# Kernel tuning notes

Hardware: AMD Instinct MI355X
Metric: run time of the kernel (lower is better)

The kernel has to match this reference:

```python
import jax, jax.numpy as jnp
import numpy as np

B, T, C, H = 8, 2048, 1024, 64  # batch, seq_len, num_embed, size_head


def setup_inputs() -> dict:
    key = jax.random.key(0)
    kx, kq, kk, kv = jax.random.split(key, 4)
    return {
        "x": jax.random.normal(kx, (B, T, C), dtype=jnp.float32),
        "Wq": jax.random.normal(kq, (C, H), dtype=jnp.float32) * 0.02,
        "Wk": jax.random.normal(kk, (C, H), dtype=jnp.float32) * 0.02,
        "Wv": jax.random.normal(kv, (C, H), dtype=jnp.float32) * 0.02,
    }


def reference(x, Wq, Wk, Wv):
    # x: [B, T, C]; single-head causal self-attention.
    # NOTE: original scales by num_channels = x.shape[-1] (= C), not head dim.
    num_channels = x.shape[-1]
    q = jnp.einsum("btc,ch->bth", x, Wq)
    k = jnp.einsum("btc,ch->bth", x, Wk)
    v = jnp.einsum("btc,ch->bth", x, Wv)
    w = jnp.einsum("bqh,bkh->bqk", q, k) * (num_channels ** -0.5)  # [B,T,T]
    causal = jnp.tril(jnp.ones((x.shape[1], x.shape[1]), dtype=bool))
    w = jnp.where(causal, w, -jnp.inf)
    w = jax.nn.softmax(w, axis=-1)
    # dropout is identity in eval/reference mode
    out = jnp.einsum("bqk,bkh->bqh", w, v)  # [B,T,H]
    return out
```

## Files before the change

kernel.cpp:

```cpp
#include <hip/hip_runtime.h>
#include <hip/hip_bf16.h>
#include <stdint.h>

#define Bn 8
#define Tn 2048
#define Cn 1024
#define Hn 64

typedef __attribute__((ext_vector_type(8))) short bf16x8;
typedef __attribute__((ext_vector_type(4))) short bf16x4;
typedef __attribute__((ext_vector_type(4))) float f32x4;

#if defined(__HIP_DEVICE_COMPILE__) && !__has_builtin(__builtin_amdgcn_mfma_f32_16x16x16bf16_1k)
#error "mfma_f32_16x16x16bf16_1k required on gfx950"
#endif
#define MFMA16(a, b, c) __builtin_amdgcn_mfma_f32_16x16x16bf16_1k(a, b, c, 0, 0, 0)
#define MFMA32(a, b, c) __builtin_amdgcn_mfma_f32_16x16x32_bf16(a, b, c, 0, 0, 0)

__device__ __forceinline__ unsigned short f2bf(float f) {
  union { float f; unsigned int u; } v; v.f = f;
  unsigned int u = v.u;
  u = u + 0x7fffu + ((u >> 16) & 1u);
  return (unsigned short)(u >> 16);
}

__device__ __forceinline__ void gload16(const void* g, void* l) {
  __builtin_amdgcn_global_load_lds(
      (const __attribute__((address_space(1))) unsigned int*)g,
      (__attribute__((address_space(3))) unsigned int*)l, 16, 0, 0);
}

__global__ __launch_bounds__(256) void k_prep(const float* __restrict__ Wq,
                                              const float* __restrict__ Wk,
                                              const float* __restrict__ Wv,
                                              unsigned short* __restrict__ Wt) {
  const int m = blockIdx.x >> 6;
  const int h = blockIdx.x & 63;
  const float* W = (m == 0) ? Wq : (m == 1) ? Wk : Wv;
  const int tid = threadIdx.x;
  unsigned short* dst = Wt + ((size_t)(m * 64 + h)) * 1024;
#pragma unroll
  for (int j = 0; j < 4; ++j) {
    int c = j * 256 + tid;
    dst[c] = f2bf(W[(size_t)c * 64 + h]);
  }
}

__global__ __launch_bounds__(256, 2) void k_qkv(const float* __restrict__ x,
                                                const unsigned short* __restrict__ Wt,
                                                unsigned short* __restrict__ Q,
                                                unsigned short* __restrict__ K,
                                                unsigned short* __restrict__ Vt) {
  __shared__ __align__(16) char smem[32256];
  unsigned short (*xs)[72] = (unsigned short (*)[72])smem;
  unsigned short (*wsh)[72] = (unsigned short (*)[72])(smem + 32 * 72 * 2);
  unsigned short (*os)[200] = (unsigned short (*)[200])smem;

  const int tid = threadIdx.x;
  const int lane = tid & 63;
  const int wid = tid >> 6;
  const int wm = wid >> 1, wn = wid & 1;
  const int l15 = lane & 15, g = lane >> 4;
  const int r0 = blockIdx.x * 32;

  f32x4 acc[6];
#pragma unroll
  for (int j = 0; j < 6; ++j)
#pragma unroll
    for (int r = 0; r < 4; ++r) acc[j][r] = 0.f;

  const int srow = tid >> 3;
  const int scol = (tid & 7) * 8;

  for (int kt = 0; kt < 16; ++kt) {
    const int k0 = kt * 64;
    const float* xp = x + (size_t)(r0 + srow) * 1024 + k0 + scol;
    {
      float4 v0 = *(const float4*)xp;
      float4 v1 = *(const float4*)(xp + 4);
      ushort4 b0, b1;
      b0.x = f2bf(v0.x); b0.y = f2bf(v0.y); b0.z = f2bf(v0.z); b0.w = f2bf(v0.w);
      b1.x = f2bf(v1.x); b1.y = f2bf(v1.y); b1.z = f2bf(v1.z); b1.w = f2bf(v1.w);
      *(ushort4*)&xs[srow][scol] = b0;
      *(ushort4*)&xs[srow][scol + 4] = b1;
    }
#pragma unroll
    for (int j = 0; j < 6; ++j) {
      int u = j * 256 + tid;
      int row = u >> 3, ch = u & 7;
      uint4 w = *(const uint4*)(Wt + (size_t)row * 1024 + k0 + ch * 8);
      *(uint4*)&wsh[row][ch * 8] = w;
    }
    __syncthreads();
#pragma unroll
    for (int kf = 0; kf < 2; ++kf) {
      bf16x8 a = *(const bf16x8*)&xs[wm * 16 + l15][kf * 32 + g * 8];
#pragma unroll
      for (int nf = 0; nf < 6; ++nf) {
        bf16x8 bfr = *(const bf16x8*)&wsh[wn * 96 + nf * 16 + l15][kf * 32 + g * 8];
        acc[nf] = MFMA32(a, bfr, acc[nf]);
      }
    }
    __syncthreads();
  }

#pragma unroll
  for (int nf = 0; nf < 6; ++nf)
#pragma unroll
    for (int r = 0; r < 4; ++r)
      os[wm * 16 + 4 * g + r][wn * 96 + nf * 16 + l15] = f2bf(acc[nf][r]);
  __syncthreads();

  const int b = r0 >> 11;
  const int t0 = r0 & 2047;
  {
    int row = tid >> 3, ch = tid & 7;
    *(uint4*)(Q + (size_t)(r0 + row) * 64 + ch * 8) = *(const uint4*)&os[row][ch * 8];
    *(uint4*)(K + (size_t)(r0 + row) * 64 + ch * 8) = *(const uint4*)&os[row][64 + ch * 8];
  }
  {
    int h = tid >> 2, tc = (tid & 3) * 8;
    unsigned short tmp[8];
#pragma unroll
    for (int r = 0; r < 8; ++r) tmp[r] = os[tc + r][128 + h];
    *(uint4*)(Vt + ((size_t)b * 64 + h) * 2048 + t0 + tc) = *(const uint4*)tmp;
  }
}

__global__ __launch_bounds__(256, 3) void k_attn_coop(const unsigned short* __restrict__ Q,
                                                      const unsigned short* __restrict__ K,
                                                      const unsigned short* __restrict__ Vt,
                                                      float* __restrict__ out,
                                                      float* __restrict__ po,
                                                      float* __restrict__ pml) {
  __shared__ __align__(16) unsigned short lds[2][8192];

  const int tid = threadIdx.x;
  const int lane = tid & 63;
  const int l15 = lane & 15, g = lane >> 4;
  const int wid = __builtin_amdgcn_readfirstlane(tid >> 6);

  const int raw = blockIdx.x;
  const int bi = (raw & 7) * 144 + (raw >> 3);
  const int b = bi / 144;
  const int id = bi - b * 144;
  int gq = 0;
#pragma unroll
  for (int t = 1; t < 8; ++t)
    if (id >= 2 * t * (t + 1)) gq = t;
  const int rem = id - 2 * gq * (gq + 1);
  const int ql = rem / (gq + 1);
  const int s = rem - ql * (gq + 1);
  const int qt = 4 * gq + ql;
  const int qblk = qt * 64;
  const int klo = 256 * s;
  const int khi = min(klo + 256, qblk + 64);
  const int nt = (khi - klo + 63) >> 6;
  const int q0w = qblk + wid * 16;

  const unsigned short* Qb = Q + (size_t)b * Tn * Hn;
  const unsigned short* Kb = K + (size_t)b * Tn * Hn;
  const unsigned short* Vb = Vt + (size_t)b * Hn * Tn;

  bf16x8 bq0 = *(const bf16x8*)(Qb + (size_t)(q0w + l15) * 64 + g * 8);
  bf16x8 bq1 = *(const bf16x8*)(Qb + (size_t)(q0w + l15) * 64 + 32 + g * 8);

  f32x4 o[4];
#pragma unroll
  for (int hf = 0; hf < 4; ++hf)
#pragma unroll
    for (int r = 0; r < 4; ++r) o[hf][r] = 0.f;
  float m = -1e30f, lsum = 0.f;
  const float sc = 0.03125f * 1.44269504088896f;

  auto stage = [&](int buf, int k0) {
    unsigned short* tb = &lds[buf][0];
#pragma unroll
    for (int j = 0; j < 4; ++j) {
      const int p = wid * 256 + j * 64 + lane;
      const unsigned short* src;
      if (wid < 2) {
        const int row = p >> 3, c = p & 7;
        src = Kb + (size_t)(k0 + row) * 64 + ((c ^ (row & 7)) * 8);
      } else {
        const int q = p - 512;
        const int h = q >> 3, c = q & 7;
        src = Vb + (size_t)h * Tn + k0 + ((c ^ (h & 7)) * 8);
      }
      gload16(src, tb + wid * 2048 + j * 512);
    }
  };

  stage(0, klo);
  __syncthreads();

  for (int t = 0; t < nt; ++t) {
    const int cur = t & 1;
    const int k0 = klo + t * 64;
    if (t + 1 < nt) stage(cur ^ 1, klo + (t + 1) * 64);

    const unsigned short* kt = &lds[cur][0];
    const unsigned short* vt = &lds[cur][4096];

    f32x4 sacc[4];
#pragma unroll
    for (int kc = 0; kc < 4; ++kc) {
      const int row = kc * 16 + l15;
      const int sw = row & 7;
      bf16x8 ka = *(const bf16x8*)&kt[row * 64 + ((g ^ sw) * 8)];
      bf16x8 kb2 = *(const bf16x8*)&kt[row * 64 + (((4 + g) ^ sw) * 8)];
#pragma unroll
      for (int r = 0; r < 4; ++r) sacc[kc][r] = 0.f;
      sacc[kc] = MFMA32(ka, bq0, sacc[kc]);
      sacc[kc] = MFMA32(kb2, bq1, sacc[kc]);
    }
    float sv[4][4];
    if (k0 + 63 > q0w) {
      const int q = q0w + l15;
#pragma unroll
      for (int kc = 0; kc < 4; ++kc)
#pragma unroll
        for (int r = 0; r < 4; ++r) {
          int key = k0 + kc * 16 + 4 * g + r;
          sv[kc][r] = (key <= q) ? sacc[kc][r] * sc : -1e30f;
        }
    } else {
#pragma unroll
      for (int kc = 0; kc < 4; ++kc)
#pragma unroll
        for (int r = 0; r < 4; ++r) sv[kc][r] = sacc[kc][r] * sc;
    }
    float pm = sv[0][0];
#pragma unroll
    for (int kc = 0; kc < 4; ++kc)
#pragma unroll
      for (int r = 0; r < 4; ++r) pm = fmaxf(pm, sv[kc][r]);
    if (__any(pm > m + 8.f)) {
      pm = fmaxf(pm, __shfl_xor(pm, 16));
      pm = fmaxf(pm, __shfl_xor(pm, 32));
      float mn = fmaxf(m, pm);
      float alpha = exp2f(m - mn);
      lsum *= alpha;
      float an[4];
#pragma unroll
      for (int r = 0; r < 4; ++r) an[r] = __shfl(alpha, 4 * g + r);
#pragma unroll
      for (int hf = 0; hf < 4; ++hf)
#pragma unroll
        for (int r = 0; r < 4; ++r) o[hf][r] *= an[r];
      m = mn;
    }
    float ts = 0.f;
#pragma unroll
    for (int kc = 0; kc < 4; ++kc)
#pragma unroll
      for (int r = 0; r < 4; ++r) { sv[kc][r] = exp2f(sv[kc][r] - m); ts += sv[kc][r]; }
    ts += __shfl_xor(ts, 16);
    ts += __shfl_xor(ts, 32);
    lsum += ts;
    bf16x4 pa[4];
#pragma unroll
    for (int kc = 0; kc < 4; ++kc) {
      pa[kc][0] = (short)f2bf(sv[kc][0]); pa[kc][1] = (short)f2bf(sv[kc][1]);
      pa[kc][2] = (short)f2bf(sv[kc][2]); pa[kc][3] = (short)f2bf(sv[kc][3]);
    }
    bf16x4 vf[4][4];
#pragma unroll
    for (int hf = 0; hf < 4; ++hf) {
      const int h = hf * 16 + l15, hs = h & 7;
#pragma unroll
      for (int kc = 0; kc < 4; ++kc) {
        const int gran = (kc * 2 + (g >> 1)) ^ hs;
        vf[hf][kc] = *(const bf16x4*)&vt[h * 64 + gran * 8 + (g & 1) * 4];
      }
    }
#pragma unroll
    for (int hf = 0; hf < 4; ++hf)
#pragma unroll
      for (int kc = 0; kc < 4; ++kc)
        o[hf] = MFMA16(pa[kc], vf[hf][kc], o[hf]);

    __syncthreads();
  }

  if (qt >= 4) {
    const int slot = b * 140 + id - 4;
    float* pob = po + (size_t)slot * 4096;
#pragma unroll
    for (int hf = 0; hf < 4; ++hf)
#pragma unroll
      for (int r = 0; r < 4; ++r)
        pob[(16 * wid + 4 * g + r) * 64 + hf * 16 + l15] = o[hf][r];
    if (lane < 16) {
      pml[(size_t)slot * 128 + 16 * wid + l15] = m;
      pml[(size_t)slot * 128 + 64 + 16 * wid + l15] = lsum;
    }
  } else {
    const float il = 1.f / lsum;
    float iln[4];
#pragma unroll
    for (int r = 0; r < 4; ++r) iln[r] = __shfl(il, 4 * g + r);
    float* ob = out + ((size_t)b * Tn + q0w) * 64;
#pragma unroll
    for (int hf = 0; hf < 4; ++hf)
#pragma unroll
      for (int r = 0; r < 4; ++r)
        ob[(size_t)(4 * g + r) * 64 + hf * 16 + l15] = o[hf][r] * iln[r];
  }
}

__global__ __launch_bounds__(256) void k_comb(const float* __restrict__ po,
                                              const float* __restrict__ pml,
                                              float* __restrict__ out) {
  const int qt = 4 + blockIdx.x;
  const int b = blockIdx.y;
  const int gq = qt >> 2, ql = qt & 3;
  const int nseg = gq + 1;
  const int base = b * 140 + 2 * gq * (gq + 1) + ql * (gq + 1) - 4;
  const int r = threadIdx.x >> 2;
  const int cg = threadIdx.x & 3;

  float mv[8], lv[8], M = -1e30f;
#pragma unroll
  for (int s = 0; s < 8; ++s)
    if (s < nseg) {
      mv[s] = pml[(size_t)(base + s) * 128 + r];
      lv[s] = pml[(size_t)(base + s) * 128 + 64 + r];
      M = fmaxf(M, mv[s]);
    }
  float w[8], L = 0.f;
#pragma unroll
  for (int s = 0; s < 8; ++s)
    if (s < nseg) { w[s] = exp2f(mv[s] - M); L += w[s] * lv[s]; }

  float acc[16];
#pragma unroll
  for (int c = 0; c < 16; ++c) acc[c] = 0.f;
#pragma unroll
  for (int s = 0; s < 8; ++s)
    if (s < nseg) {
      const float* pb = po + (size_t)(base + s) * 4096 + r * 64 + cg * 16;
#pragma unroll
      for (int j = 0; j < 4; ++j) {
        float4 v = *(const float4*)(pb + 4 * j);
        acc[4 * j + 0] += w[s] * v.x; acc[4 * j + 1] += w[s] * v.y;
        acc[4 * j + 2] += w[s] * v.z; acc[4 * j + 3] += w[s] * v.w;
      }
    }
  const float invL = 1.f / L;
  float* ob = out + ((size_t)b * Tn + qt * 64 + r) * 64 + cg * 16;
#pragma unroll
  for (int j = 0; j < 4; ++j) {
    float4 v;
    v.x = acc[4 * j + 0] * invL; v.y = acc[4 * j + 1] * invL;
    v.z = acc[4 * j + 2] * invL; v.w = acc[4 * j + 3] * invL;
    *(float4*)(ob + 4 * j) = v;
  }
}

__global__ __launch_bounds__(256, 2) void k_attn_wave(const unsigned short* __restrict__ Q,
                                                      const unsigned short* __restrict__ K,
                                                      const unsigned short* __restrict__ Vt,
                                                      float* __restrict__ out) {
  const int tid = threadIdx.x;
  const int lane = tid & 63;
  const int l15 = lane & 15, g = lane >> 4;
  const int wid = tid >> 6;
  const int task = blockIdx.x * 4 + wid;
  const int b = task >> 7, qt = task & 127;
  const int q0 = qt * 16;
  const int nt = (q0 + 16 + 63) >> 6;

  const unsigned short* Qb = Q + (size_t)b * Tn * Hn;
  const unsigned short* Kb = K + (size_t)b * Tn * Hn;
  const unsigned short* Vb = Vt + (size_t)b * Hn * Tn;

  bf16x8 bq0 = *(const bf16x8*)(Qb + (size_t)(q0 + l15) * 64 + g * 8);
  bf16x8 bq1 = *(const bf16x8*)(Qb + (size_t)(q0 + l15) * 64 + 32 + g * 8);

  f32x4 o[4];
#pragma unroll
  for (int hf = 0; hf < 4; ++hf)
#pragma unroll
    for (int r = 0; r < 4; ++r) o[hf][r] = 0.f;
  float m = -1e30f, lsum = 0.f;
  const float sc = 0.03125f * 1.44269504088896f;

  for (int t = 0; t < nt; ++t) {
    const int k0 = t * 64;
    bf16x4 vf[4][4];
#pragma unroll
    for (int hf = 0; hf < 4; ++hf) {
      const unsigned short* vrow = Vb + (size_t)(hf * 16 + l15) * Tn + k0 + 4 * g;
#pragma unroll
      for (int kc = 0; kc < 4; ++kc) vf[hf][kc] = *(const bf16x4*)(vrow + kc * 16);
    }
    f32x4 sacc[4];
#pragma unroll
    for (int kc = 0; kc < 4; ++kc) {
      const unsigned short* kp = Kb + (size_t)(k0 + kc * 16 + l15) * 64 + g * 8;
      bf16x8 ka = *(const bf16x8*)kp;
      bf16x8 kb2 = *(const bf16x8*)(kp + 32);
#pragma unroll
      for (int r = 0; r < 4; ++r) sacc[kc][r] = 0.f;
      sacc[kc] = MFMA32(ka, bq0, sacc[kc]);
      sacc[kc] = MFMA32(kb2, bq1, sacc[kc]);
    }
    float sv[4][4];
    if (k0 + 63 > q0) {
      const int q = q0 + l15;
#pragma unroll
      for (int kc = 0; kc < 4; ++kc)
#pragma unroll
        for (int r = 0; r < 4; ++r) {
          int key = k0 + kc * 16 + 4 * g + r;
          sv[kc][r] = (key <= q) ? sacc[kc][r] * sc : -1e30f;
        }
    } else {
#pragma unroll
      for (int kc = 0; kc < 4; ++kc)
#pragma unroll
        for (int r = 0; r < 4; ++r) sv[kc][r] = sacc[kc][r] * sc;
    }
    float pm = sv[0][0];
#pragma unroll
    for (int kc = 0; kc < 4; ++kc)
#pragma unroll
      for (int r = 0; r < 4; ++r) pm = fmaxf(pm, sv[kc][r]);
    if (__any(pm > m + 8.f)) {
      pm = fmaxf(pm, __shfl_xor(pm, 16));
      pm = fmaxf(pm, __shfl_xor(pm, 32));
      float mn = fmaxf(m, pm);
      float alpha = exp2f(m - mn);
      lsum *= alpha;
      float an[4];
#pragma unroll
      for (int r = 0; r < 4; ++r) an[r] = __shfl(alpha, 4 * g + r);
#pragma unroll
      for (int hf = 0; hf < 4; ++hf)
#pragma unroll
        for (int r = 0; r < 4; ++r) o[hf][r] *= an[r];
      m = mn;
    }
    float ts = 0.f;
#pragma unroll
    for (int kc = 0; kc < 4; ++kc)
#pragma unroll
      for (int r = 0; r < 4; ++r) { sv[kc][r] = exp2f(sv[kc][r] - m); ts += sv[kc][r]; }
    ts += __shfl_xor(ts, 16);
    ts += __shfl_xor(ts, 32);
    lsum += ts;
    bf16x4 pa[4];
#pragma unroll
    for (int kc = 0; kc < 4; ++kc) {
      pa[kc][0] = (short)f2bf(sv[kc][0]); pa[kc][1] = (short)f2bf(sv[kc][1]);
      pa[kc][2] = (short)f2bf(sv[kc][2]); pa[kc][3] = (short)f2bf(sv[kc][3]);
    }
#pragma unroll
    for (int hf = 0; hf < 4; ++hf)
#pragma unroll
      for (int kc = 0; kc < 4; ++kc)
        o[hf] = MFMA16(pa[kc], vf[hf][kc], o[hf]);
  }
  const float il = 1.f / lsum;
  float iln[4];
#pragma unroll
  for (int r = 0; r < 4; ++r) iln[r] = __shfl(il, 4 * g + r);
  float* ob = out + ((size_t)b * Tn + q0) * 64;
#pragma unroll
  for (int hf = 0; hf < 4; ++hf)
#pragma unroll
    for (int r = 0; r < 4; ++r)
      ob[(size_t)(4 * g + r) * 64 + hf * 16 + l15] = o[hf][r] * iln[r];
}

extern "C" void kernel_launch(void* const* d_in, const int* in_sizes, int n_in,
                              void* d_out, int out_size, void* d_ws, size_t ws_size,
                              hipStream_t stream) {
  const float* x  = (const float*)d_in[0];
  const float* Wq = (const float*)d_in[1];
  const float* Wk = (const float*)d_in[2];
  const float* Wv = (const float*)d_in[3];
  float* out = (float*)d_out;

  unsigned short* Wt = (unsigned short*)d_ws;
  unsigned short* Qs = Wt + 3 * 64 * 1024;
  unsigned short* Ks = Qs + (size_t)Bn * Tn * Hn;
  unsigned short* Vt = Ks + (size_t)Bn * Tn * Hn;
  const size_t bf_bytes = (3 * 64 * 1024 + 3 * (size_t)Bn * Tn * Hn) * 2;
  float* po = (float*)((char*)d_ws + bf_bytes);

  const size_t nslots = (size_t)Bn * 140;
  float* pml = po + nslots * 4096;
  const size_t need = bf_bytes + nslots * (4096 + 128) * sizeof(float);

  hipLaunchKernelGGL(k_prep, dim3(192), dim3(256), 0, stream, Wq, Wk, Wv, Wt);
  hipLaunchKernelGGL(k_qkv, dim3(512), dim3(256), 0, stream, x, Wt, Qs, Ks, Vt);
  if (ws_size >= need) {
    hipLaunchKernelGGL(k_attn_coop, dim3(1152), dim3(256), 0, stream, Qs, Ks, Vt, out, po, pml);
    hipLaunchKernelGGL(k_comb, dim3(28, 8), dim3(256), 0, stream, po, pml, out);
  } else {
    hipLaunchKernelGGL(k_attn_wave, dim3(256), dim3(256), 0, stream, Qs, Ks, Vt, out);
  }
}
```

Before: 54.93 us.

## Load QKV projection operands directly from global memory into MFMA registers

The QKV projection kernel no longer stages x and weight tiles through shared memory with two barriers per k-step. Each wave instead reads its MFMA fragments straight from global memory, converts x to bf16 in registers, and computes a 32x48 output tile over a fully unrolled k loop. This is meant to remove LDS traffic and synchronisation. In exchange, each x row is now read by all four waves, so global and L2 traffic goes up. The fragment loads are also strided and less coalesced.

```diff
diff --git a/kernel.cpp b/kernel.cpp
--- a/kernel.cpp
+++ b/kernel.cpp
@@ -51,64 +51,62 @@
                                                 unsigned short* __restrict__ Q,
                                                 unsigned short* __restrict__ K,
                                                 unsigned short* __restrict__ Vt) {
-  __shared__ __align__(16) char smem[32256];
-  unsigned short (*xs)[72] = (unsigned short (*)[72])smem;
-  unsigned short (*wsh)[72] = (unsigned short (*)[72])(smem + 32 * 72 * 2);
-  unsigned short (*os)[200] = (unsigned short (*)[200])smem;
+  __shared__ __align__(16) unsigned short os[32][200];
 
   const int tid = threadIdx.x;
   const int lane = tid & 63;
   const int wid = tid >> 6;
-  const int wm = wid >> 1, wn = wid & 1;
   const int l15 = lane & 15, g = lane >> 4;
   const int r0 = blockIdx.x * 32;
 
-  f32x4 acc[6];
-#pragma unroll
-  for (int j = 0; j < 6; ++j)
-#pragma unroll
-    for (int r = 0; r < 4; ++r) acc[j][r] = 0.f;
-
-  const int srow = tid >> 3;
-  const int scol = (tid & 7) * 8;
-
-  for (int kt = 0; kt < 16; ++kt) {
-    const int k0 = kt * 64;
-    const float* xp = x + (size_t)(r0 + srow) * 1024 + k0 + scol;
-    {
-      float4 v0 = *(const float4*)xp;
-      float4 v1 = *(const float4*)(xp + 4);
-      ushort4 b0, b1;
-      b0.x = f2bf(v0.x); b0.y = f2bf(v0.y); b0.z = f2bf(v0.z); b0.w = f2bf(v0.w);
-      b1.x = f2bf(v1.x); b1.y = f2bf(v1.y); b1.z = f2bf(v1.z); b1.w = f2bf(v1.w);
-      *(ushort4*)&xs[srow][scol] = b0;
-      *(ushort4*)&xs[srow][scol + 4] = b1;
-    }
-#pragma unroll
-    for (int j = 0; j < 6; ++j) {
-      int u = j * 256 + tid;
-      int row = u >> 3, ch = u & 7;
-      uint4 w = *(const uint4*)(Wt + (size_t)row * 1024 + k0 + ch * 8);
-      *(uint4*)&wsh[row][ch * 8] = w;
-    }
-    __syncthreads();
-#pragma unroll
-    for (int kf = 0; kf < 2; ++kf) {
-      bf16x8 a = *(const bf16x8*)&xs[wm * 16 + l15][kf * 32 + g * 8];
-#pragma unroll
-      for (int nf = 0; nf < 6; ++nf) {
-        bf16x8 bfr = *(const bf16x8*)&wsh[wn * 96 + nf * 16 + l15][kf * 32 + g * 8];
-        acc[nf] = MFMA32(a, bfr, acc[nf]);
-      }
-    }
-    __syncthreads();
-  }
-
-#pragma unroll
-  for (int nf = 0; nf < 6; ++nf)
-#pragma unroll
-    for (int r = 0; r < 4; ++r)
-      os[wm * 16 + 4 * g + r][wn * 96 + nf * 16 + l15] = f2bf(acc[nf][r]);
+  f32x4 acc[2][3];
+#pragma unroll
+  for (int mf = 0; mf < 2; ++mf)
+#pragma unroll
+    for (int nf = 0; nf < 3; ++nf)
+#pragma unroll
+      for (int r = 0; r < 4; ++r) acc[mf][nf][r] = 0.f;
+
+  const float* xr0 = x + (size_t)(r0 + l15) * 1024 + g * 8;
+  const float* xr1 = x + (size_t)(r0 + 16 + l15) * 1024 + g * 8;
+  const unsigned short* wr0 = Wt + (size_t)(wid * 48 + l15) * 1024 + g * 8;
+  const unsigned short* wr1 = wr0 + 16 * 1024;
+  const unsigned short* wr2 = wr0 + 32 * 1024;
+
+#pragma unroll
+  for (int ks = 0; ks < 32; ++ks) {
+    const int k0 = ks * 32;
+    float4 a0l = *(const float4*)(xr0 + k0);
+    float4 a0h = *(const float4*)(xr0 + k0 + 4);
+    float4 a1l = *(const float4*)(xr1 + k0);
+    float4 a1h = *(const float4*)(xr1 + k0 + 4);
+    bf16x8 a0, a1;
+    a0[0] = (short)f2bf(a0l.x); a0[1] = (short)f2bf(a0l.y);
+    a0[2] = (short)f2bf(a0l.z); a0[3] = (short)f2bf(a0l.w);
+    a0[4] = (short)f2bf(a0h.x); a0[5] = (short)f2bf(a0h.y);
+    a0[6] = (short)f2bf(a0h.z); a0[7] = (short)f2bf(a0h.w);
+    a1[0] = (short)f2bf(a1l.x); a1[1] = (short)f2bf(a1l.y);
+    a1[2] = (short)f2bf(a1l.z); a1[3] = (short)f2bf(a1l.w);
+    a1[4] = (short)f2bf(a1h.x); a1[5] = (short)f2bf(a1h.y);
+    a1[6] = (short)f2bf(a1h.z); a1[7] = (short)f2bf(a1h.w);
+    bf16x8 b0 = *(const bf16x8*)(wr0 + k0);
+    bf16x8 b1 = *(const bf16x8*)(wr1 + k0);
+    bf16x8 b2 = *(const bf16x8*)(wr2 + k0);
+    acc[0][0] = MFMA32(a0, b0, acc[0][0]);
+    acc[0][1] = MFMA32(a0, b1, acc[0][1]);
+    acc[0][2] = MFMA32(a0, b2, acc[0][2]);
+    acc[1][0] = MFMA32(a1, b0, acc[1][0]);
+    acc[1][1] = MFMA32(a1, b1, acc[1][1]);
+    acc[1][2] = MFMA32(a1, b2, acc[1][2]);
+  }
+
+#pragma unroll
+  for (int mf = 0; mf < 2; ++mf)
+#pragma unroll
+    for (int nf = 0; nf < 3; ++nf)
+#pragma unroll
+      for (int r = 0; r < 4; ++r)
+        os[mf * 16 + 4 * g + r][wid * 48 + nf * 16 + l15] = f2bf(acc[mf][nf][r]);
   __syncthreads();
 
   const int b = r0 >> 11;
```

Result: slower. 86.57 us (+57.6%).

## Double-buffer QKV projection with larger 64-row tiles and swizzled async W loads

Applied to the files above, without the earlier changes.

Restructures the QKV projection kernel to use 512-thread blocks over 64 rows with a 128-wide K step. Each wave now computes a 2x3 MFMA fragment grid instead of 1x6. X and W tiles are double-buffered in a large LDS allocation. The next tile's W is staged with direct global-to-LDS loads using an XOR swizzle against bank conflicts, overlapping loads with the current MFMAs. This halves the number of blocks and repeated W fetches, at the cost of one block per CU and heavy LDS use.

```diff
diff --git a/kernel.cpp b/kernel.cpp
--- a/kernel.cpp
+++ b/kernel.cpp
@@ -46,69 +46,97 @@
   }
 }
 
-__global__ __launch_bounds__(256, 2) void k_qkv(const float* __restrict__ x,
+__global__ __launch_bounds__(512, 1) void k_qkv(const float* __restrict__ x,
                                                 const unsigned short* __restrict__ Wt,
                                                 unsigned short* __restrict__ Q,
                                                 unsigned short* __restrict__ K,
                                                 unsigned short* __restrict__ Vt) {
-  __shared__ __align__(16) char smem[32256];
-  unsigned short (*xs)[72] = (unsigned short (*)[72])smem;
-  unsigned short (*wsh)[72] = (unsigned short (*)[72])(smem + 32 * 72 * 2);
-  unsigned short (*os)[200] = (unsigned short (*)[200])smem;
+  __shared__ __align__(16) char smem[133120];
 
   const int tid = threadIdx.x;
   const int lane = tid & 63;
-  const int wid = tid >> 6;
-  const int wm = wid >> 1, wn = wid & 1;
+  const int wid = __builtin_amdgcn_readfirstlane(tid >> 6);
+  const int wm = wid >> 2, wn = wid & 3;
   const int l15 = lane & 15, g = lane >> 4;
-  const int r0 = blockIdx.x * 32;
-
-  f32x4 acc[6];
-#pragma unroll
-  for (int j = 0; j < 6; ++j)
-#pragma unroll
-    for (int r = 0; r < 4; ++r) acc[j][r] = 0.f;
-
-  const int srow = tid >> 3;
-  const int scol = (tid & 7) * 8;
-
-  for (int kt = 0; kt < 16; ++kt) {
-    const int k0 = kt * 64;
-    const float* xp = x + (size_t)(r0 + srow) * 1024 + k0 + scol;
-    {
-      float4 v0 = *(const float4*)xp;
-      float4 v1 = *(const float4*)(xp + 4);
-      ushort4 b0, b1;
-      b0.x = f2bf(v0.x); b0.y = f2bf(v0.y); b0.z = f2bf(v0.z); b0.w = f2bf(v0.w);
-      b1.x = f2bf(v1.x); b1.y = f2bf(v1.y); b1.z = f2bf(v1.z); b1.w = f2bf(v1.w);
-      *(ushort4*)&xs[srow][scol] = b0;
-      *(ushort4*)&xs[srow][scol + 4] = b1;
-    }
+  const int r0 = blockIdx.x * 64;
+
+  f32x4 acc[2][3];
+#pragma unroll
+  for (int mf = 0; mf < 2; ++mf)
+#pragma unroll
+    for (int nf = 0; nf < 3; ++nf)
+#pragma unroll
+      for (int r = 0; r < 4; ++r) acc[mf][nf][r] = 0.f;
+
+  auto stageW = [&](int buf, int kt) {
+    char* wl = smem + 34816 + buf * 49152;
+    const int k0 = kt * 128;
 #pragma unroll
     for (int j = 0; j < 6; ++j) {
-      int u = j * 256 + tid;
-      int row = u >> 3, ch = u & 7;
-      uint4 w = *(const uint4*)(Wt + (size_t)row * 1024 + k0 + ch * 8);
-      *(uint4*)&wsh[row][ch * 8] = w;
+      const int cidx = wid + j * 8;
+      const int row = cidx * 4 + (lane >> 4);
+      const int lg = (lane & 15) ^ (row & 15);
+      gload16(Wt + (size_t)row * 1024 + k0 + lg * 8, wl + cidx * 1024);
+    }
+  };
+  auto stageX = [&](int buf, int kt) {
+    unsigned short (*xs)[136] = (unsigned short (*)[136])(smem + buf * 17408);
+    const int row = tid >> 3;
+    const int c0 = (tid & 7) * 16;
+    const float* xp = x + (size_t)(r0 + row) * 1024 + kt * 128 + c0;
+    float4 v0 = *(const float4*)xp;
+    float4 v1 = *(const float4*)(xp + 4);
+    float4 v2 = *(const float4*)(xp + 8);
+    float4 v3 = *(const float4*)(xp + 12);
+    ushort4 b0, b1, b2, b3;
+    b0.x = f2bf(v0.x); b0.y = f2bf(v0.y); b0.z = f2bf(v0.z); b0.w = f2bf(v0.w);
+    b1.x = f2bf(v1.x); b1.y = f2bf(v1.y); b1.z = f2bf(v1.z); b1.w = f2bf(v1.w);
+    b2.x = f2bf(v2.x); b2.y = f2bf(v2.y); b2.z = f2bf(v2.z); b2.w = f2bf(v2.w);
+    b3.x = f2bf(v3.x); b3.y = f2bf(v3.y); b3.z = f2bf(v3.z); b3.w = f2bf(v3.w);
+    *(ushort4*)&xs[row][c0] = b0;
+    *(ushort4*)&xs[row][c0 + 4] = b1;
+    *(ushort4*)&xs[row][c0 + 8] = b2;
+    *(ushort4*)&xs[row][c0 + 12] = b3;
+  };
+
+  stageW(0, 0);
+  stageX(0, 0);
+  __syncthreads();
+
+  for (int kt = 0; kt < 8; ++kt) {
+    const int cur = kt & 1;
+    if (kt < 7) {
+      stageW(cur ^ 1, kt + 1);
+      stageX(cur ^ 1, kt + 1);
+    }
+    const unsigned short (*xs)[136] =
+        (const unsigned short (*)[136])(smem + cur * 17408);
+    const unsigned short* wl = (const unsigned short*)(smem + 34816 + cur * 49152);
+#pragma unroll
+    for (int ks = 0; ks < 4; ++ks) {
+      bf16x8 a0 = *(const bf16x8*)&xs[wm * 32 + l15][ks * 32 + g * 8];
+      bf16x8 a1 = *(const bf16x8*)&xs[wm * 32 + 16 + l15][ks * 32 + g * 8];
+#pragma unroll
+      for (int nf = 0; nf < 3; ++nf) {
+        const int row = wn * 48 + nf * 16 + l15;
+        const int phys = (ks * 4 + g) ^ (row & 15);
+        bf16x8 b = *(const bf16x8*)&wl[row * 128 + phys * 8];
+        acc[0][nf] = MFMA32(a0, b, acc[0][nf]);
+        acc[1][nf] = MFMA32(a1, b, acc[1][nf]);
+      }
     }
     __syncthreads();
-#pragma unroll
-    for (int kf = 0; kf < 2; ++kf) {
-      bf16x8 a = *(const bf16x8*)&xs[wm * 16 + l15][kf * 32 + g * 8];
-#pragma unroll
-      for (int nf = 0; nf < 6; ++nf) {
-        bf16x8 bfr = *(const bf16x8*)&wsh[wn * 96 + nf * 16 + l15][kf * 32 + g * 8];
-        acc[nf] = MFMA32(a, bfr, acc[nf]);
-      }
-    }
-    __syncthreads();
-  }
-
-#pragma unroll
-  for (int nf = 0; nf < 6; ++nf)
-#pragma unroll
-    for (int r = 0; r < 4; ++r)
-      os[wm * 16 + 4 * g + r][wn * 96 + nf * 16 + l15] = f2bf(acc[nf][r]);
+  }
+
+  unsigned short (*os)[200] = (unsigned short (*)[200])smem;
+#pragma unroll
+  for (int mf = 0; mf < 2; ++mf)
+#pragma unroll
+    for (int nf = 0; nf < 3; ++nf)
+#pragma unroll
+      for (int r = 0; r < 4; ++r)
+        os[wm * 32 + mf * 16 + 4 * g + r][wn * 48 + nf * 16 + l15] =
+            f2bf(acc[mf][nf][r]);
   __syncthreads();
 
   const int b = r0 >> 11;
@@ -119,7 +147,7 @@
     *(uint4*)(K + (size_t)(r0 + row) * 64 + ch * 8) = *(const uint4*)&os[row][64 + ch * 8];
   }
   {
-    int h = tid >> 2, tc = (tid & 3) * 8;
+    int h = tid >> 3, tc = (tid & 7) * 8;
     unsigned short tmp[8];
 #pragma unroll
     for (int r = 0; r < 8; ++r) tmp[r] = os[tc + r][128 + h];
@@ -495,7 +523,7 @@
   const size_t need = bf_bytes + nslots * (4096 + 128) * sizeof(float);
 
   hipLaunchKernelGGL(k_prep, dim3(192), dim3(256), 0, stream, Wq, Wk, Wv, Wt);
-  hipLaunchKernelGGL(k_qkv, dim3(512), dim3(256), 0, stream, x, Wt, Qs, Ks, Vt);
+  hipLaunchKernelGGL(k_qkv, dim3(256), dim3(512), 0, stream, x, Wt, Qs, Ks, Vt);
   if (ws_size >= need) {
     hipLaunchKernelGGL(k_attn_coop, dim3(1152), dim3(256), 0, stream, Qs, Ks, Vt, out, po, pml);
     hipLaunchKernelGGL(k_comb, dim3(28, 8), dim3(256), 0, stream, po, pml, out);
```

New measurement: 57.36 us. 4.4% more time.
